# Performance work log

Hardware: AMD Instinct MI355X
Metric: run time of the kernel (lower is better)

The kernel has to match this reference:

```python
import jax, jax.numpy as jnp
import numpy as np

HEAD_DIM = 32
KERNEL = 3
DILATION = 2
PAD = DILATION * (KERNEL - 1) // 2  # = 2
SCALE = HEAD_DIM ** (-0.5)


def _unfold(x):
    """Emulate nn.Unfold(kernel_size=KERNEL, dilation=DILATION, padding=PAD, stride=1).
    x: [B, C, H, W] -> [B, C, K*K, H, W] (channel-major, kernel positions inner,
    matching torch's C*K*K channel layout after the module's reshape)."""
    B, C, H, W = x.shape
    xp = jnp.pad(x, ((0, 0), (0, 0), (PAD, PAD), (PAD, PAD)))
    patches = [xp[:, :, i * DILATION:i * DILATION + H, j * DILATION:j * DILATION + W]
               for i in range(KERNEL) for j in range(KERNEL)]
    return jnp.stack(patches, axis=2)  # [B, C, K2, H, W]


def setup_inputs() -> dict:
    key = jax.random.key(0)
    kq, kk, kv = jax.random.split(key, 3)
    B, d, H, W = 4, 384, 64, 64
    q = jax.random.normal(kq, (B, d, H, W), dtype=jnp.float32)
    k = jax.random.normal(kk, (B, d, H, W), dtype=jnp.float32)
    v = jax.random.normal(kv, (B, d, H, W), dtype=jnp.float32)
    return {"q": q, "k": k, "v": v}


def reference(q, k, v):
    B, d, H, W = q.shape
    nh = d // HEAD_DIM
    K2 = KERNEL * KERNEL
    L = H * W
    # q: [B, nh, hd, L]
    qh = q.reshape(B, nh, HEAD_DIM, L)
    # unfolded k, v: [B, nh, hd, K2, L]
    ku = _unfold(k).reshape(B, nh, HEAD_DIM, K2, L)
    vu = _unfold(v).reshape(B, nh, HEAD_DIM, K2, L)
    # per-pixel attention logits: [B, nh, L, K2]
    attn = jnp.einsum('bncl,bnckl->bnlk', qh, ku) * SCALE
    attn = jax.nn.softmax(attn, axis=-1)
    # weighted values: [B, nh, L, hd]
    out = jnp.einsum('bnlk,bnckl->bnlc', attn, vu)
    # -> [B, L, nh, hd] -> [B, H, W, d]
    return out.transpose(0, 2, 1, 3).reshape(B, H, W, d)
```

## Files before the change

### kernel.cpp

```cpp
#include <hip/hip_runtime.h>
#include <hip/hip_bf16.h>


#define HD   32
#define NHD  12
#define DDIM 384
#define HH   64
#define WW   64
#define HWSZ 4096
#define SCALEF 0.17677669529663687f

__global__ __launch_bounds__(256) void dilate_attn(const float* __restrict__ q,
                                                   const float* __restrict__ k,
                                                   const float* __restrict__ v,
                                                   float* __restrict__ out) {
    const int tid = threadIdx.x;
    const int r   = tid >> 6;
    const int x   = tid & 63;
    const int bz  = blockIdx.x;
    const int bh  = bz >> 4;
    const int b   = bh / NHD;
    const int n   = bh - b * NHD;
    const int y   = (bz & 15) * 4 + r;

    const size_t chan_base = (size_t)(b * DDIM + n * HD) * HWSZ;
    const int pix = y * WW + x;

    int  toff[9];
    bool tval[9];
#pragma unroll
    for (int di = 0; di < 3; ++di) {
        int yy = y + 2 * di - 2;
        bool vy = (yy >= 0) && (yy < HH);
#pragma unroll
        for (int p = 0; p < 3; ++p) {
            int xo = x + 2 * p - 2;
            bool vx = (xo >= 0) && (xo < WW);
            bool ok = vy && vx;
            tval[di * 3 + p] = ok;
            toff[di * 3 + p] = ok ? (yy * WW + xo) : pix;
        }
    }

    const float* qb = q + chan_base + pix;
    float qreg[HD];
#pragma unroll
    for (int c = 0; c < HD; ++c) qreg[c] = qb[(size_t)c * HWSZ] * SCALEF;

    const float* kbase = k + chan_base;
    float l[9];
#pragma unroll
    for (int t = 0; t < 9; ++t) {
        const float* kt = kbase + toff[t];
        float a0 = 0.f, a1 = 0.f;
#pragma unroll
        for (int c = 0; c < HD; c += 2) {
            a0 += qreg[c]     * kt[(size_t)c * HWSZ];
            a1 += qreg[c + 1] * kt[(size_t)(c + 1) * HWSZ];
        }
        float acc = a0 + a1;
        l[t] = tval[t] ? acc : 0.f;
    }

    float m = l[0];
#pragma unroll
    for (int t = 1; t < 9; ++t) m = fmaxf(m, l[t]);
    float w[9], s = 0.f;
#pragma unroll
    for (int t = 0; t < 9; ++t) { w[t] = __expf(l[t] - m); s += w[t]; }
    float inv = 1.0f / s;
#pragma unroll
    for (int t = 0; t < 9; ++t) w[t] = tval[t] ? (w[t] * inv) : 0.f;

    const float* vbase = v + chan_base;
    float* ob = out + ((size_t)(b * HH + y) * WW + x) * DDIM + n * HD;

#pragma unroll
    for (int half = 0; half < 2; ++half) {
        const float* vh = vbase + (size_t)(half * 16) * HWSZ;
        float o[16];
#pragma unroll
        for (int c = 0; c < 16; ++c) o[c] = 0.f;
#pragma unroll
        for (int t = 0; t < 9; ++t) {
            const float* vt = vh + toff[t];
            float wt = w[t];
#pragma unroll
            for (int c = 0; c < 16; ++c) o[c] += wt * vt[(size_t)c * HWSZ];
        }
        float* oh = ob + half * 16;
        *(float4*)(oh)      = make_float4(o[0],  o[1],  o[2],  o[3]);
        *(float4*)(oh + 4)  = make_float4(o[4],  o[5],  o[6],  o[7]);
        *(float4*)(oh + 8)  = make_float4(o[8],  o[9],  o[10], o[11]);
        *(float4*)(oh + 12) = make_float4(o[12], o[13], o[14], o[15]);
    }
}

extern "C" void kernel_launch(void* const* d_in, const int* in_sizes, int n_in,
                              void* d_out, int out_size, void* d_ws, size_t ws_size,
                              hipStream_t stream) {
    const float* q = (const float*)d_in[0];
    const float* k = (const float*)d_in[1];
    const float* v = (const float*)d_in[2];
    float* out = (float*)d_out;
    hipLaunchKernelGGL(dilate_attn, dim3(768), dim3(256), 0, stream, q, k, v, out);
}
```

Before: 134.1 us.

## Split head channels across four lanes with shuffle-reduced logits, swizzle blocks

Each pixel's 32 head channels are now split across four groups of 8 channels handled by different lanes in a wavefront. The partial q·k dot products are combined with cross-lane xor shuffles before the softmax. This quadruples the block count and cuts per-thread register use, with launch bounds asking for higher occupancy. A block-index swizzle spreads consecutive blocks across XCDs. In exchange, each warp now covers only 16 x-pixels per row and repeats the softmax math four times, and 32-bit index arithmetic replaces size_t.

New measurement: 194.8 us. 1.45x slower.

```diff
diff --git a/kernel.cpp b/kernel.cpp
--- a/kernel.cpp
+++ b/kernel.cpp
@@ -1,8 +1,6 @@
 #include <hip/hip_runtime.h>
-#include <hip/hip_bf16.h>
 
 
-#define HD   32
 #define NHD  12
 #define DDIM 384
 #define HH   64
@@ -10,21 +8,25 @@
 #define HWSZ 4096
 #define SCALEF 0.17677669529663687f
 
-__global__ __launch_bounds__(256) void dilate_attn(const float* __restrict__ q,
-                                                   const float* __restrict__ k,
-                                                   const float* __restrict__ v,
-                                                   float* __restrict__ out) {
+__global__ __launch_bounds__(256, 6) void dilate_attn(const float* __restrict__ q,
+                                                      const float* __restrict__ k,
+                                                      const float* __restrict__ v,
+                                                      float* __restrict__ out) {
     const int tid = threadIdx.x;
-    const int r   = tid >> 6;
-    const int x   = tid & 63;
-    const int bz  = blockIdx.x;
-    const int bh  = bz >> 4;
-    const int b   = bh / NHD;
-    const int n   = bh - b * NHD;
-    const int y   = (bz & 15) * 4 + r;
+    const int xl  = tid & 15;
+    const int cg  = (tid >> 4) & 3;
+    const int x   = ((tid >> 6) << 4) | xl;
 
-    const size_t chan_base = (size_t)(b * DDIM + n * HD) * HWSZ;
-    const int pix = y * WW + x;
+    int bz = blockIdx.x;
+    bz = (bz & 7) * 384 + (bz >> 3);
+
+    const int y  = bz & 63;
+    const int bh = bz >> 6;
+    const int b  = bh / NHD;
+    const int n  = bh - b * NHD;
+
+    const int cbase = (b * DDIM + n * 32 + cg * 8) * HWSZ;
+    const int pix   = y * WW + x;
 
     int  toff[9];
     bool tval[9];
@@ -35,31 +37,33 @@
 #pragma unroll
         for (int p = 0; p < 3; ++p) {
             int xo = x + 2 * p - 2;
-            bool vx = (xo >= 0) && (xo < WW);
-            bool ok = vy && vx;
+            bool ok = vy && (xo >= 0) && (xo < WW);
             tval[di * 3 + p] = ok;
             toff[di * 3 + p] = ok ? (yy * WW + xo) : pix;
         }
     }
 
-    const float* qb = q + chan_base + pix;
-    float qreg[HD];
+    float qreg[8];
 #pragma unroll
-    for (int c = 0; c < HD; ++c) qreg[c] = qb[(size_t)c * HWSZ] * SCALEF;
+    for (int c = 0; c < 8; ++c) qreg[c] = q[cbase + pix + c * HWSZ] * SCALEF;
 
-    const float* kbase = k + chan_base;
     float l[9];
 #pragma unroll
     for (int t = 0; t < 9; ++t) {
-        const float* kt = kbase + toff[t];
+        const int kb = cbase + toff[t];
         float a0 = 0.f, a1 = 0.f;
 #pragma unroll
-        for (int c = 0; c < HD; c += 2) {
-            a0 += qreg[c]     * kt[(size_t)c * HWSZ];
-            a1 += qreg[c + 1] * kt[(size_t)(c + 1) * HWSZ];
+        for (int c = 0; c < 8; c += 2) {
+            a0 += qreg[c]     * k[kb + c * HWSZ];
+            a1 += qreg[c + 1] * k[kb + (c + 1) * HWSZ];
         }
-        float acc = a0 + a1;
-        l[t] = tval[t] ? acc : 0.f;
+        l[t] = tval[t] ? (a0 + a1) : 0.f;
+    }
+
+#pragma unroll
+    for (int t = 0; t < 9; ++t) {
+        l[t] += __shfl_xor(l[t], 16, 64);
+        l[t] += __shfl_xor(l[t], 32, 64);
     }
 
     float m = l[0];
@@ -72,28 +76,20 @@
 #pragma unroll
     for (int t = 0; t < 9; ++t) w[t] = tval[t] ? (w[t] * inv) : 0.f;
 
-    const float* vbase = v + chan_base;
-    float* ob = out + ((size_t)(b * HH + y) * WW + x) * DDIM + n * HD;
+    float o[8];
+#pragma unroll
+    for (int c = 0; c < 8; ++c) o[c] = 0.f;
+#pragma unroll
+    for (int t = 0; t < 9; ++t) {
+        const int vb = cbase + toff[t];
+        float wt = w[t];
+#pragma unroll
+        for (int c = 0; c < 8; ++c) o[c] += wt * v[vb + c * HWSZ];
+    }
 
-#pragma unroll
-    for (int half = 0; half < 2; ++half) {
-        const float* vh = vbase + (size_t)(half * 16) * HWSZ;
-        float o[16];
-#pragma unroll
-        for (int c = 0; c < 16; ++c) o[c] = 0.f;
-#pragma unroll
-        for (int t = 0; t < 9; ++t) {
-            const float* vt = vh + toff[t];
-            float wt = w[t];
-#pragma unroll
-            for (int c = 0; c < 16; ++c) o[c] += wt * vt[(size_t)c * HWSZ];
-        }
-        float* oh = ob + half * 16;
-        *(float4*)(oh)      = make_float4(o[0],  o[1],  o[2],  o[3]);
-        *(float4*)(oh + 4)  = make_float4(o[4],  o[5],  o[6],  o[7]);
-        *(float4*)(oh + 8)  = make_float4(o[8],  o[9],  o[10], o[11]);
-        *(float4*)(oh + 12) = make_float4(o[12], o[13], o[14], o[15]);
-    }
+    const int ob = ((b * HH + y) * WW + x) * DDIM + n * 32 + cg * 8;
+    *(float4*)(out + ob)     = make_float4(o[0], o[1], o[2], o[3]);
+    *(float4*)(out + ob + 4) = make_float4(o[4], o[5], o[6], o[7]);
 }
 
 extern "C" void kernel_launch(void* const* d_in, const int* in_sizes, int n_in,
@@ -103,5 +99,5 @@
     const float* k = (const float*)d_in[1];
     const float* v = (const float*)d_in[2];
     float* out = (float*)d_out;
-    hipLaunchKernelGGL(dilate_attn, dim3(768), dim3(256), 0, stream, q, k, v, out);
+    hipLaunchKernelGGL(dilate_attn, dim3(3072), dim3(256), 0, stream, q, k, v, out);
 }
```
